# Optimization experiments

Measured on AMD Instinct MI355X. Metric: run time of the kernel, lower is better.

Reference implementation:

```python
import jax, jax.numpy as jnp
import numpy as np

V, BS, L, H, D, DF = 32000, 2048, 4, 4, 256, 1024
B, T = 2, 2048
DH = D // H


def setup_inputs() -> dict:
    key = jax.random.key(0)
    ks = iter(jax.random.split(key, 32))
    s = 0.02
    rn = lambda shape: jax.random.normal(next(ks), shape, jnp.float32) * s
    inp = {
        'idx': jax.random.randint(next(ks), (B, T), 0, V),
        'tok_emb': rn((V, D)),
        'pos_emb': rn((BS, D)),
        'Wq': rn((L, D, D)), 'bq': jnp.zeros((L, D)),
        'Wk': rn((L, D, D)), 'bk': jnp.zeros((L, D)),
        'Wv': rn((L, D, D)), 'bv': jnp.zeros((L, D)),
        'Wo': rn((L, D, D)), 'bo': jnp.zeros((L, D)),
        'ln1_g': jnp.ones((L, D)), 'ln1_b': jnp.zeros((L, D)),
        'W1': rn((L, D, DF)), 'b1': jnp.zeros((L, DF)),
        'W2': rn((L, DF, D)), 'b2': jnp.zeros((L, D)),
        'ln2_g': jnp.ones((L, D)), 'ln2_b': jnp.zeros((L, D)),
        'lnf_g': jnp.ones((D,)), 'lnf_b': jnp.zeros((D,)),
        'head_W': rn((D, V)), 'head_b': jnp.zeros((V,)),
    }
    return inp


def _layernorm(x, g, b, eps=1e-5):
    mu = jnp.mean(x, axis=-1, keepdims=True)
    var = jnp.mean(jnp.square(x - mu), axis=-1, keepdims=True)
    return (x - mu) * jax.lax.rsqrt(var + eps) * g + b


def reference(idx, tok_emb, pos_emb, Wq, bq, Wk, bk, Wv, bv, Wo, bo,
              ln1_g, ln1_b, W1, b1, W2, b2, ln2_g, ln2_b,
              lnf_g, lnf_b, head_W, head_b):
    b, t = idx.shape
    x = tok_emb[idx] + pos_emb[:t]  # [B,T,D]
    causal = jnp.tril(jnp.ones((t, t), dtype=bool))  # [T,T]
    scale = 1.0 / np.sqrt(DH)
    neg_inf = jnp.finfo(x.dtype).min
    for l in range(L):
        h = _layernorm(x, ln1_g[l], ln1_b[l])
        q = (h @ Wq[l] + bq[l]).reshape(b, t, H, DH)
        k = (h @ Wk[l] + bk[l]).reshape(b, t, H, DH)
        v = (h @ Wv[l] + bv[l]).reshape(b, t, H, DH)
        att = jnp.einsum('bqhd,bkhd->bhqk', q, k) * scale
        att = jnp.where(causal, att, neg_inf)
        att = jax.nn.softmax(att, axis=-1)
        y = jnp.einsum('bhqk,bkhd->bqhd', att, v).reshape(b, t, D)
        x = x + (y @ Wo[l] + bo[l])
        h = _layernorm(x, ln2_g[l], ln2_b[l])
        x = x + (jax.nn.gelu(h @ W1[l] + b1[l], approximate=False) @ W2[l] + b2[l])
    x = _layernorm(x, lnf_g, lnf_b)
    return x @ head_W + head_b  # [B,T,V]
```

## Files before the change

kernel.cpp:

```cpp
#include <hip/hip_runtime.h>
#include <hip/hip_bf16.h>
#include <math.h>

#define V_   32000
#define L_   4
#define H_   4
#define D_   256
#define DF_  1024
#define B_   2
#define T_   2048
#define DH_  64
#define NTOK (B_*T_)

typedef __attribute__((ext_vector_type(8))) short bf16x8;
typedef __attribute__((ext_vector_type(4))) float f32x4;
typedef unsigned short u16;

#define GLOAD16(gsrc, ldst) \
  __builtin_amdgcn_global_load_lds((const __attribute__((address_space(1))) void*)(gsrc), \
                                   (__attribute__((address_space(3))) void*)(ldst), 16, 0, 0)

__device__ __forceinline__ u16 f2bf(float f) {
    unsigned int u = __builtin_bit_cast(unsigned int, f);
    u = (u + 0x7fff + ((u >> 16) & 1)) >> 16;
    return (u16)u;
}

__device__ __forceinline__ int xcd_swizzle(int orig, int nwg) {
    return ((nwg & 7) == 0) ? ((orig & 7) * (nwg >> 3) + (orig >> 3)) : orig;
}

__global__ __launch_bounds__(256) void prep_kernel(
    const float* __restrict__ Wq, const float* __restrict__ Wk,
    const float* __restrict__ Wv, const float* __restrict__ Wo,
    const float* __restrict__ W1, const float* __restrict__ W2,
    const float* __restrict__ hW,
    u16* __restrict__ WqkvT, u16* __restrict__ WoT,
    u16* __restrict__ W1T, u16* __restrict__ W2T, u16* __restrict__ hWT)
{
    int b = blockIdx.x;
    const float* src; u16* dst; int K, N, k0, n0;
    if (b < 512) {
        int m = b >> 5, t = b & 31;
        int wt = m & 3, l = m >> 2;
        K = 256; N = 256;
        src = (wt == 0 ? Wq : wt == 1 ? Wk : wt == 2 ? Wv : Wo) + (size_t)l * 65536;
        dst = (wt < 3) ? WqkvT + (size_t)l * 196608 + (size_t)wt * 65536
                       : WoT + (size_t)l * 65536;
        k0 = (t >> 3) * 64; n0 = (t & 7) * 32;
    } else if (b < 1024) {
        int bb = b - 512; int l = bb >> 7, t = bb & 127;
        K = 256; N = 1024;
        src = W1 + (size_t)l * 262144; dst = W1T + (size_t)l * 262144;
        k0 = (t >> 5) * 64; n0 = (t & 31) * 32;
    } else if (b < 1536) {
        int bb = b - 1024; int l = bb >> 7, t = bb & 127;
        K = 1024; N = 256;
        src = W2 + (size_t)l * 262144; dst = W2T + (size_t)l * 262144;
        k0 = (t >> 3) * 64; n0 = (t & 7) * 32;
    } else {
        int bb = b - 1536;
        K = 256; N = 32000;
        src = hW; dst = hWT;
        k0 = (bb / 1000) * 64; n0 = (bb % 1000) * 32;
    }
    __shared__ float tile[64][33];
    int tid = threadIdx.x;
    int tc = tid & 31, tr = tid >> 5;
    #pragma unroll
    for (int i = 0; i < 8; i++)
        tile[tr + i*8][tc] = src[(size_t)(k0 + tr + i*8) * N + n0 + tc];
    __syncthreads();
    int kc = tid & 63, nr = tid >> 6;
    #pragma unroll
    for (int i = 0; i < 8; i++)
        dst[(size_t)(n0 + nr + i*4) * K + k0 + kc] = f2bf(tile[kc][nr + i*4]);
}

__global__ __launch_bounds__(256) void embed_qkv_kernel(
    const int* __restrict__ idx, const float* __restrict__ tok, const float* __restrict__ pos,
    const float* __restrict__ g, const float* __restrict__ bta,
    const u16* __restrict__ WqkvT0,
    const float* __restrict__ bq, const float* __restrict__ bk, const float* __restrict__ bv,
    float* __restrict__ x, u16* __restrict__ qkv)
{
    __shared__ u16 Bs[2][256*64];
    __shared__ u16 hS[16][264];

    int tid = threadIdx.x;
    int lane = tid & 63, w = tid >> 6;
    int lr = lane & 15, lg = lane >> 4;
    int bid = xcd_swizzle(blockIdx.x, 256);
    int row0 = bid * 16;

    {
        int grow = tid >> 4;
        int gcol = (tid & 15) * 16;
        int n = row0 + grow;
        int t = n & (T_ - 1);
        int id = idx[n];
        float vv[16];
        #pragma unroll
        for (int i = 0; i < 4; i++) {
            float4 a = *(const float4*)(tok + (size_t)id * D_ + gcol + i * 4);
            float4 b = *(const float4*)(pos + (size_t)t * D_ + gcol + i * 4);
            vv[i*4+0] = a.x + b.x; vv[i*4+1] = a.y + b.y;
            vv[i*4+2] = a.z + b.z; vv[i*4+3] = a.w + b.w;
        }
        float s = 0.f, q = 0.f;
        #pragma unroll
        for (int i = 0; i < 16; i++) { s += vv[i]; q += vv[i]*vv[i]; }
        #pragma unroll
        for (int o = 1; o <= 8; o <<= 1) { s += __shfl_xor(s, o); q += __shfl_xor(q, o); }
        float mu = s * (1.0f / D_);
        float var = q * (1.0f / D_) - mu * mu;
        float ri = rsqrtf(var + 1e-5f);
        #pragma unroll
        for (int i = 0; i < 16; i++) {
            x[(size_t)n * D_ + gcol + i] = vv[i];
            hS[grow][gcol + i] = f2bf((vv[i] - mu) * ri * g[gcol + i] + bta[gcol + i]);
        }
    }

    auto stageQ = [&](int buf, int u) {
        const u16* BT = WqkvT0 + (size_t)(u >> 2) * 65536;
        int k0 = (u & 3) * 64;
        #pragma unroll
        for (int i = 0; i < 8; i++) {
            int o16 = tid + i * 256;
            int r = o16 >> 3;
            int sw = ((o16 & 7) << 4) ^ ((r & 7) << 4);
            GLOAD16(BT + (size_t)r * 256 + k0 + (sw >> 1), &Bs[buf][o16 * 8]);
        }
    };
    auto afH = [&](int t, int ks) -> bf16x8 {
        return *(const bf16x8*)(&hS[lr][(t * 128 + ks * 64 + lg * 16) >> 1]);
    };
    auto bfr = [&](int buf, int ni, int ks) -> bf16x8 {
        int rr = w * 64 + ni * 16 + lr;
        return *(const bf16x8*)(&Bs[buf][rr * 64 + (((ks * 64 + lg * 16) ^ ((rr & 7) << 4)) >> 1)]);
    };

    stageQ(0, 0);
    f32x4 acc[4] = {};
    for (int u = 0; u < 12; u++) {
        __syncthreads();
        if (u + 1 < 12) stageQ((u + 1) & 1, u + 1);
        int t = u & 3;
        #pragma unroll
        for (int ks = 0; ks < 2; ks++) {
            bf16x8 a = afH(t, ks);
            __builtin_amdgcn_s_setprio(1);
            #pragma unroll
            for (int ni = 0; ni < 4; ni++)
                acc[ni] = __builtin_amdgcn_mfma_f32_16x16x32_bf16(a, bfr(u & 1, ni, ks), acc[ni], 0, 0, 0);
            __builtin_amdgcn_s_setprio(0);
        }
        if (t == 3) {
            int sel = u >> 2;
            const float* bp = sel == 0 ? bq : sel == 1 ? bk : bv;
            #pragma unroll
            for (int ni = 0; ni < 4; ni++) {
                #pragma unroll
                for (int j = 0; j < 4; j++) {
                    int row = row0 + lg * 4 + j;
                    int cc = w * 64 + ni * 16 + lr;
                    float v = acc[ni][j] + bp[cc];
                    int bb = row >> 11, tt = row & (T_ - 1);
                    int hh = cc >> 6, dh = cc & 63;
                    qkv[(size_t)sel * NTOK * D_ +
                        ((((size_t)bb * H_ + hh) * T_) + tt) * DH_ + dh] = f2bf(v);
                }
                acc[ni] = (f32x4){0.f, 0.f, 0.f, 0.f};
            }
        }
    }
}

__global__ __launch_bounds__(256) void wo_ln_kernel(
    const u16* __restrict__ ybuf, const u16* __restrict__ WoT, const float* __restrict__ bo,
    const float* __restrict__ ln2g, const float* __restrict__ ln2b,
    float* __restrict__ x, u16* __restrict__ hbuf)
{
    __shared__ u16 As[2][16*64];
    __shared__ u16 Bs[2][256*64];
    __shared__ float sred[4][16], qred[4][16];

    int tid = threadIdx.x;
    int lane = tid & 63, w = tid >> 6;
    int lr = lane & 15, lg = lane >> 4;
    int bid = xcd_swizzle(blockIdx.x, 256);
    int row0 = bid * 16;

    auto stage = [&](int buf, int k0) {
        #pragma unroll
        for (int i = 0; i < 8; i++) {
            int o16 = tid + i * 256;
            int r = o16 >> 3;
            int sw = ((o16 & 7) << 4) ^ ((r & 7) << 4);
            GLOAD16(WoT + (size_t)r * 256 + k0 + (sw >> 1), &Bs[buf][o16 * 8]);
        }
        if (tid < 128) {
            int r = tid >> 3;
            int sw = ((tid & 7) << 4) ^ ((r & 7) << 4);
            GLOAD16(ybuf + (size_t)(row0 + r) * 256 + k0 + (sw >> 1), &As[buf][tid * 8]);
        }
    };
    auto afA = [&](int buf, int ks) -> bf16x8 {
        return *(const bf16x8*)(&As[buf][lr * 64 + (((ks * 64 + lg * 16) ^ ((lr & 7) << 4)) >> 1)]);
    };
    auto bfr = [&](int buf, int ni, int ks) -> bf16x8 {
        int rr = w * 64 + ni * 16 + lr;
        return *(const bf16x8*)(&Bs[buf][rr * 64 + (((ks * 64 + lg * 16) ^ ((rr & 7) << 4)) >> 1)]);
    };

    stage(0, 0);
    f32x4 acc[4] = {};
    for (int t = 0; t < 4; t++) {
        __syncthreads();
        if (t + 1 < 4) stage((t + 1) & 1, (t + 1) * 64);
        #pragma unroll
        for (int ks = 0; ks < 2; ks++) {
            bf16x8 a = afA(t & 1, ks);
            __builtin_amdgcn_s_setprio(1);
            #pragma unroll
            for (int ni = 0; ni < 4; ni++)
                acc[ni] = __builtin_amdgcn_mfma_f32_16x16x32_bf16(a, bfr(t & 1, ni, ks), acc[ni], 0, 0, 0);
            __builtin_amdgcn_s_setprio(0);
        }
    }

    float vals[4][4];
    float rs[4] = {0,0,0,0}, rq[4] = {0,0,0,0};
    #pragma unroll
    for (int ni = 0; ni < 4; ni++)
        #pragma unroll
        for (int j = 0; j < 4; j++) {
            int row = row0 + lg * 4 + j;
            int col = w * 64 + ni * 16 + lr;
            float v = acc[ni][j] + bo[col] + x[(size_t)row * D_ + col];
            x[(size_t)row * D_ + col] = v;
            vals[ni][j] = v;
            rs[j] += v; rq[j] += v * v;
        }
    #pragma unroll
    for (int j = 0; j < 4; j++)
        #pragma unroll
        for (int o = 1; o <= 8; o <<= 1) { rs[j] += __shfl_xor(rs[j], o); rq[j] += __shfl_xor(rq[j], o); }
    if (lr == 0)
        #pragma unroll
        for (int j = 0; j < 4; j++) { sred[w][lg*4 + j] = rs[j]; qred[w][lg*4 + j] = rq[j]; }
    __syncthreads();
    #pragma unroll
    for (int j = 0; j < 4; j++) {
        int r = lg * 4 + j;
        float mu = (sred[0][r] + sred[1][r] + sred[2][r] + sred[3][r]) * (1.0f / D_);
        float var = (qred[0][r] + qred[1][r] + qred[2][r] + qred[3][r]) * (1.0f / D_) - mu * mu;
        float ri = rsqrtf(var + 1e-5f);
        int row = row0 + r;
        #pragma unroll
        for (int ni = 0; ni < 4; ni++) {
            int col = w * 64 + ni * 16 + lr;
            hbuf[(size_t)row * D_ + col] = f2bf((vals[ni][j] - mu) * ri * ln2g[col] + ln2b[col]);
        }
    }
}

__global__ __launch_bounds__(256) void ff1_kernel(
    const u16* __restrict__ A, const u16* __restrict__ BT,
    const float* __restrict__ bias, u16* __restrict__ C)
{
    __shared__ u16 As[2][64*64];
    __shared__ u16 Bs[2][64*64];
    int tid = threadIdx.x;
    int lane = tid & 63, w = tid >> 6;
    int lr = lane & 15, lg = lane >> 4;
    int wm = w >> 1, wn = w & 1;

    int gx = gridDim.x;
    int nwg = gx * gridDim.y;
    int orig = blockIdx.y * gx + blockIdx.x;
    int bid = xcd_swizzle(orig, nwg);
    int row0 = (bid / gx) * 64, col0 = (bid % gx) * 64;

    auto stage = [&](int buf, int k0) {
        #pragma unroll
        for (int i = 0; i < 2; i++) {
            int o16 = tid + i * 256;
            int r = o16 >> 3;
            int sw = ((o16 & 7) << 4) ^ ((r & 7) << 4);
            GLOAD16(A + (size_t)(row0 + r) * 256 + k0 + (sw >> 1), &As[buf][o16 * 8]);
            GLOAD16(BT + (size_t)(col0 + r) * 256 + k0 + (sw >> 1), &Bs[buf][o16 * 8]);
        }
    };

    stage(0, 0);
    f32x4 acc[2][2] = {};
    for (int t = 0; t < 4; t++) {
        __syncthreads();
        if (t + 1 < 4) stage((t + 1) & 1, (t + 1) * 64);
        #pragma unroll
        for (int ks = 0; ks < 2; ks++) {
            bf16x8 af[2], bfv[2];
            #pragma unroll
            for (int mi = 0; mi < 2; mi++) {
                int rr = wm * 32 + mi * 16 + lr;
                af[mi] = *(const bf16x8*)(&As[t & 1][rr * 64 + (((ks * 64 + lg * 16) ^ ((rr & 7) << 4)) >> 1)]);
            }
            #pragma unroll
            for (int ni = 0; ni < 2; ni++) {
                int rr = wn * 32 + ni * 16 + lr;
                bfv[ni] = *(const bf16x8*)(&Bs[t & 1][rr * 64 + (((ks * 64 + lg * 16) ^ ((rr & 7) << 4)) >> 1)]);
            }
            __builtin_amdgcn_s_setprio(1);
            #pragma unroll
            for (int mi = 0; mi < 2; mi++)
                #pragma unroll
                for (int ni = 0; ni < 2; ni++)
                    acc[mi][ni] = __builtin_amdgcn_mfma_f32_16x16x32_bf16(af[mi], bfv[ni], acc[mi][ni], 0, 0, 0);
            __builtin_amdgcn_s_setprio(0);
        }
    }

    #pragma unroll
    for (int mi = 0; mi < 2; mi++)
        #pragma unroll
        for (int ni = 0; ni < 2; ni++)
            #pragma unroll
            for (int j = 0; j < 4; j++) {
                int row = row0 + wm * 32 + mi * 16 + lg * 4 + j;
                int col = col0 + wn * 32 + ni * 16 + lr;
                float v = acc[mi][ni][j] + bias[col];
                v = 0.5f * v * (1.0f + erff(v * 0.70710678118f));
                C[(size_t)row * DF_ + col] = f2bf(v);
            }
}

template<bool LAST>
__global__ __launch_bounds__(256) void ff2qkv_kernel(
    const u16* __restrict__ ff, const u16* __restrict__ W2T, const float* __restrict__ b2,
    const float* __restrict__ lng, const float* __restrict__ lnb,
    const u16* __restrict__ WqkvT,
    const float* __restrict__ bq, const float* __restrict__ bk, const float* __restrict__ bv,
    float* __restrict__ x, u16* __restrict__ hout, u16* __restrict__ qkv)
{
    __shared__ u16 As[2][16*64];
    __shared__ u16 Bs[2][256*64];
    __shared__ u16 hS[16][264];
    __shared__ float sred[4][16], qred[4][16];

    int tid = threadIdx.x;
    int lane = tid & 63, w = tid >> 6;
    int lr = lane & 15, lg = lane >> 4;
    int bid = xcd_swizzle(blockIdx.x, 256);
    int row0 = bid * 16;

    auto stageB = [&](int buf, const u16* BT, int K, int k0) {
        #pragma unroll
        for (int i = 0; i < 8; i++) {
            int o16 = tid + i * 256;
            int r = o16 >> 3;
            int sw = ((o16 & 7) << 4) ^ ((r & 7) << 4);
            GLOAD16(BT + (size_t)r * K + k0 + (sw >> 1), &Bs[buf][o16 * 8]);
        }
    };
    auto stageA = [&](int buf, int k0) {
        if (tid < 128) {
            int r = tid >> 3;
            int sw = ((tid & 7) << 4) ^ ((r & 7) << 4);
            GLOAD16(ff + (size_t)(row0 + r) * DF_ + k0 + (sw >> 1), &As[buf][tid * 8]);
        }
    };
    auto prefetch = [&](int u) {
        if (u < 16) { stageA(u & 1, u * 64); stageB(u & 1, W2T, 1024, u * 64); }
        else if (!LAST && u < 28) {
            int v = u - 16;
            stageB(u & 1, WqkvT + (size_t)(v >> 2) * 65536, 256, (v & 3) * 64);
        }
    };
    auto afA = [&](int buf, int ks) -> bf16x8 {
        return *(const bf16x8*)(&As[buf][lr * 64 + (((ks * 64 + lg * 16) ^ ((lr & 7) << 4)) >> 1)]);
    };
    auto afH = [&](int t, int ks) -> bf16x8 {
        return *(const bf16x8*)(&hS[lr][(t * 128 + ks * 64 + lg * 16) >> 1]);
    };
    auto bfr = [&](int buf, int ni, int ks) -> bf16x8 {
        int rr = w * 64 + ni * 16 + lr;
        return *(const bf16x8*)(&Bs[buf][rr * 64 + (((ks * 64 + lg * 16) ^ ((rr & 7) << 4)) >> 1)]);
    };

    prefetch(0);
    f32x4 acc[4] = {};
    for (int u = 0; u < 16; u++) {
        __syncthreads();
        prefetch(u + 1);
        #pragma unroll
        for (int ks = 0; ks < 2; ks++) {
            bf16x8 a = afA(u & 1, ks);
            __builtin_amdgcn_s_setprio(1);
            #pragma unroll
            for (int ni = 0; ni < 4; ni++)
                acc[ni] = __builtin_amdgcn_mfma_f32_16x16x32_bf16(a, bfr(u & 1, ni, ks), acc[ni], 0, 0, 0);
            __builtin_amdgcn_s_setprio(0);
        }
    }

    {
        float vals[4][4];
        float rs[4] = {0,0,0,0}, rq[4] = {0,0,0,0};
        #pragma unroll
        for (int ni = 0; ni < 4; ni++)
            #pragma unroll
            for (int j = 0; j < 4; j++) {
                int row = row0 + lg * 4 + j;
                int col = w * 64 + ni * 16 + lr;
                float v = acc[ni][j] + b2[col] + x[(size_t)row * D_ + col];
                x[(size_t)row * D_ + col] = v;
                vals[ni][j] = v;
                rs[j] += v; rq[j] += v * v;
            }
        #pragma unroll
        for (int j = 0; j < 4; j++)
            #pragma unroll
            for (int o = 1; o <= 8; o <<= 1) { rs[j] += __shfl_xor(rs[j], o); rq[j] += __shfl_xor(rq[j], o); }
        if (lr == 0)
            #pragma unroll
            for (int j = 0; j < 4; j++) { sred[w][lg*4 + j] = rs[j]; qred[w][lg*4 + j] = rq[j]; }
        __syncthreads();
        #pragma unroll
        for (int j = 0; j < 4; j++) {
            int r = lg * 4 + j;
            float mu = (sred[0][r] + sred[1][r] + sred[2][r] + sred[3][r]) * (1.0f / D_);
            float var = (qred[0][r] + qred[1][r] + qred[2][r] + qred[3][r]) * (1.0f / D_) - mu * mu;
            float ri = rsqrtf(var + 1e-5f);
            #pragma unroll
            for (int ni = 0; ni < 4; ni++) {
                int col = w * 64 + ni * 16 + lr;
                float hv = (vals[ni][j] - mu) * ri * lng[col] + lnb[col];
                if (LAST) hout[(size_t)(row0 + r) * D_ + col] = f2bf(hv);
                else      hS[r][col] = f2bf(hv);
            }
        }
    }

    if constexpr (!LAST) {
        f32x4 accT[4] = {};
        for (int v = 0; v < 12; v++) {
            __syncthreads();
            prefetch(16 + v + 1);
            int t = v & 3;
            #pragma unroll
            for (int ks = 0; ks < 2; ks++) {
                bf16x8 a = afH(t, ks);
                __builtin_amdgcn_s_setprio(1);
                #pragma unroll
                for (int ni = 0; ni < 4; ni++)
                    accT[ni] = __builtin_amdgcn_mfma_f32_16x16x32_bf16(a, bfr(v & 1, ni, ks), accT[ni], 0, 0, 0);
                __builtin_amdgcn_s_setprio(0);
            }
            if (t == 3) {
                int sel = v >> 2;
                const float* bp = sel == 0 ? bq : sel == 1 ? bk : bv;
                #pragma unroll
                for (int ni = 0; ni < 4; ni++) {
                    #pragma unroll
                    for (int j = 0; j < 4; j++) {
                        int row = row0 + lg * 4 + j;
                        int cc = w * 64 + ni * 16 + lr;
                        float val = accT[ni][j] + bp[cc];
                        int bb = row >> 11, tt = row & (T_ - 1);
                        int hh = cc >> 6, dh = cc & 63;
                        qkv[(size_t)sel * NTOK * D_ +
                            ((((size_t)bb * H_ + hh) * T_) + tt) * DH_ + dh] = f2bf(val);
                    }
                    accT[ni] = (f32x4){0.f, 0.f, 0.f, 0.f};
                }
            }
        }
    }
}

__global__ __launch_bounds__(256) void attn_kernel(
    const u16* __restrict__ q, const u16* __restrict__ k,
    const u16* __restrict__ v, u16* __restrict__ y)
{
    int linear = blockIdx.y * gridDim.x + blockIdx.x;
    int half = linear >> 8, rem = linear & 255;
    int qt_raw = rem & 63;
    int qt = half ? 63 - qt_raw : qt_raw;
    int bh = (rem >> 6) + half * 4;
    int bidx = bh >> 2, h = bh & 3;
    const u16* qp = q + (size_t)bh * T_ * DH_;
    const u16* kp = k + (size_t)bh * T_ * DH_;
    const u16* vp = v + (size_t)bh * T_ * DH_;

    int nch = (qt + 2) >> 1;

    __shared__ u16 Qs[32*64];
    __shared__ u16 Ks[2][2][64*64];
    __shared__ u16 VT[2][64*72];
    __shared__ u16 Ps[4][16*72];

    int tid = threadIdx.x;
    int lane = tid & 63, w = tid >> 6;
    int lr = lane & 15, lg = lane >> 4;
    int p = w >> 1;
    int rh = w & 1;
    int cnt0 = (nch + 1) >> 1, cnt1 = nch >> 1;
    int mycnt = p ? cnt1 : cnt0;
    int maxit = cnt0;

    int pp = tid >> 7;
    int ppcnt = pp ? cnt1 : cnt0;
    int vkey = tid & 63;
    int vdh0 = ((tid >> 6) & 1) * 8;

    {
        int o16 = tid, r = o16 >> 3;
        int sw = ((o16 & 7) << 4) ^ ((r & 7) << 4);
        GLOAD16(qp + (size_t)(qt * 32 + r) * DH_ + (sw >> 1), &Qs[o16 * 8]);
    }
    #pragma unroll
    for (int pr = 0; pr < 2; pr++) {
        int c = min(pr, nch - 1);
        #pragma unroll
        for (int i = 0; i < 2; i++) {
            int o16 = tid + i * 256, r = o16 >> 3;
            int sw = ((o16 & 7) << 4) ^ ((r & 7) << 4);
            GLOAD16(kp + (size_t)(c * 64 + r) * DH_ + (sw >> 1), &Ks[0][pr][o16 * 8]);
        }
    }
    bf16x8 vr[4];
    {
        int c = min(pp, nch - 1);
        #pragma unroll
        for (int g = 0; g < 4; g++)
            vr[g] = *(const bf16x8*)(vp + (size_t)(c * 64 + vkey) * DH_ + vdh0 + g * 16);
    }
    __syncthreads();
    #pragma unroll
    for (int g = 0; g < 4; g++)
        #pragma unroll
        for (int e = 0; e < 8; e++)
            VT[pp][(vdh0 + g * 16 + e) * 72 + vkey] = (u16)vr[g][e];
    bf16x8 qa[2];
    #pragma unroll
    for (int ks = 0; ks < 2; ks++) {
        int rr = rh * 16 + lr;
        qa[ks] = *(const bf16x8*)(Qs + rr * 64 + (((ks * 64 + lg * 16) ^ ((rr & 7) << 4)) >> 1));
    }
    __syncthreads();

    float m[4], lden[4];
    f32x4 o[4] = {};
    #pragma unroll
    for (int j = 0; j < 4; j++) { m[j] = -1e30f; lden[j] = 0.0f; }

    for (int it = 0; it < maxit; it++) {
        int cur = it & 1;
        if (it + 1 < maxit) {
            #pragma unroll
            for (int pr = 0; pr < 2; pr++) {
                int c = min(2 * (it + 1) + pr, nch - 1);
                #pragma unroll
                for (int i = 0; i < 2; i++) {
                    int o16 = tid + i * 256, r = o16 >> 3;
                    int sw = ((o16 & 7) << 4) ^ ((r & 7) << 4);
                    GLOAD16(kp + (size_t)(c * 64 + r) * DH_ + (sw >> 1), &Ks[cur ^ 1][pr][o16 * 8]);
                }
            }
        }
        bool vnext = (it + 1 < ppcnt);
        if (vnext) {
            int c = 2 * (it + 1) + pp;
            #pragma unroll
            for (int g = 0; g < 4; g++)
                vr[g] = *(const bf16x8*)(vp + (size_t)(c * 64 + vkey) * DH_ + vdh0 + g * 16);
        }

        bool act = (it < mycnt);
        if (act) {
            int myc = 2 * it + p;
            f32x4 sc[4];
            #pragma unroll
            for (int ct = 0; ct < 4; ct++) {
                f32x4 s = {};
                __builtin_amdgcn_s_setprio(1);
                #pragma unroll
                for (int ks = 0; ks < 2; ks++) {
                    int rr = ct * 16 + lr;
                    bf16x8 kb = *(const bf16x8*)(&Ks[cur][p][rr * 64 + (((ks * 64 + lg * 16) ^ ((rr & 7) << 4)) >> 1)]);
                    s = __builtin_amdgcn_mfma_f32_16x16x32_bf16(qa[ks], kb, s, 0, 0, 0);
                }
                __builtin_amdgcn_s_setprio(0);
                sc[ct] = s;
            }
            float mloc[4];
            #pragma unroll
            for (int j = 0; j < 4; j++) mloc[j] = -1e30f;
            #pragma unroll
            for (int ct = 0; ct < 4; ct++)
                #pragma unroll
                for (int j = 0; j < 4; j++) {
                    float s = sc[ct][j] * 0.125f;
                    int key = myc * 64 + ct * 16 + lr;
                    int qrow = qt * 32 + rh * 16 + lg * 4 + j;
                    if (key > qrow) s = -1e30f;
                    sc[ct][j] = s;
                    mloc[j] = fmaxf(mloc[j], s);
                }
            #pragma unroll
            for (int j = 0; j < 4; j++) {
                mloc[j] = fmaxf(mloc[j], __shfl_xor(mloc[j], 1));
                mloc[j] = fmaxf(mloc[j], __shfl_xor(mloc[j], 2));
                mloc[j] = fmaxf(mloc[j], __shfl_xor(mloc[j], 4));
                mloc[j] = fmaxf(mloc[j], __shfl_xor(mloc[j], 8));
            }
            float f[4], rs[4];
            #pragma unroll
            for (int j = 0; j < 4; j++) {
                float nm = fmaxf(m[j], mloc[j]);
                f[j] = __expf(m[j] - nm);
                m[j] = nm;
                rs[j] = 0.0f;
            }
            #pragma unroll
            for (int ct = 0; ct < 4; ct++)
                #pragma unroll
                for (int j = 0; j < 4; j++) {
                    float pv = __expf(sc[ct][j] - m[j]);
                    rs[j] += pv;
                    Ps[w][(lg * 4 + j) * 72 + ct * 16 + lr] = f2bf(pv);
                }
            #pragma unroll
            for (int j = 0; j < 4; j++) {
                rs[j] += __shfl_xor(rs[j], 1);
                rs[j] += __shfl_xor(rs[j], 2);
                rs[j] += __shfl_xor(rs[j], 4);
                rs[j] += __shfl_xor(rs[j], 8);
                lden[j] = lden[j] * f[j] + rs[j];
            }
            #pragma unroll
            for (int dt = 0; dt < 4; dt++)
                #pragma unroll
                for (int j = 0; j < 4; j++)
                    o[dt][j] *= f[j];
            #pragma unroll
            for (int ks = 0; ks < 2; ks++) {
                bf16x8 pa = *(const bf16x8*)(&Ps[w][lr * 72 + ks * 32 + lg * 8]);
                __builtin_amdgcn_s_setprio(1);
                #pragma unroll
                for (int dt = 0; dt < 4; dt++) {
                    bf16x8 vb = *(const bf16x8*)(&VT[p][(dt * 16 + lr) * 72 + ks * 32 + lg * 8]);
                    o[dt] = __builtin_amdgcn_mfma_f32_16x16x32_bf16(pa, vb, o[dt], 0, 0, 0);
                }
                __builtin_amdgcn_s_setprio(0);
            }
        }
        __syncthreads();
        if (vnext) {
            #pragma unroll
            for (int g = 0; g < 4; g++)
                #pragma unroll
                for (int e = 0; e < 8; e++)
                    VT[pp][(vdh0 + g * 16 + e) * 72 + vkey] = (u16)vr[g][e];
        }
        __syncthreads();
    }

    float* mg = (float*)&Ks[0][0][0];
    if (p == 1) {
        int base = (rh * 64 + lane) * 24;
        #pragma unroll
        for (int dt = 0; dt < 4; dt++)
            #pragma unroll
            for (int j = 0; j < 4; j++)
                mg[base + dt * 4 + j] = o[dt][j];
        #pragma unroll
        for (int j = 0; j < 4; j++) { mg[base + 16 + j] = m[j]; mg[base + 20 + j] = lden[j]; }
    }
    __syncthreads();
    if (p == 0) {
        int base = (rh * 64 + lane) * 24;
        #pragma unroll
        for (int j = 0; j < 4; j++) {
            float m1 = mg[base + 16 + j];
            float l1 = mg[base + 20 + j];
            float mf = fmaxf(m[j], m1);
            float e0 = __expf(m[j] - mf), e1 = __expf(m1 - mf);
            float inv = 1.0f / (lden[j] * e0 + l1 * e1);
            int qrow = qt * 32 + rh * 16 + lg * 4 + j;
            size_t ybase = ((size_t)(bidx * T_ + qrow)) * D_ + h * DH_;
            #pragma unroll
            for (int dt = 0; dt < 4; dt++) {
                float of = (o[dt][j] * e0 + mg[base + dt * 4 + j] * e1) * inv;
                y[ybase + dt * 16 + lr] = f2bf(of);
            }
        }
    }
}

__global__ __launch_bounds__(256) void head_gemm(
    const u16* __restrict__ A, const u16* __restrict__ BT,
    const float* __restrict__ bias, float* __restrict__ C,
    int M, int N, int K)
{
    __shared__ u16 As[2][128*64];
    __shared__ u16 Bs[2][128*64];
    int tid = threadIdx.x;
    int lane = tid & 63, w = tid >> 6;
    int lr = lane & 15, lg = lane >> 4;
    int wm = w >> 1, wn = w & 1;

    int orig = blockIdx.y * gridDim.x + blockIdx.x;
    int bid = xcd_swizzle(orig, 8000);
    int col0 = (bid >> 5) * 128;
    int row0 = (bid & 31) * 128;

    f32x4 acc[4][4] = {};

    auto stage = [&](int buf, int k0) {
        #pragma unroll
        for (int i = 0; i < 4; i++) {
            int o16 = tid + i * 256;
            int r = o16 >> 3;
            int sw = ((o16 & 7) << 4) ^ ((r & 7) << 4);
            GLOAD16(A + (size_t)(row0 + r) * K + k0 + (sw >> 1), &As[buf][o16 * 8]);
            GLOAD16(BT + (size_t)(col0 + r) * K + k0 + (sw >> 1), &Bs[buf][o16 * 8]);
        }
    };

    stage(0, 0);
    int nk = K >> 6;
    for (int t = 0; t < nk; t++) {
        int cur = t & 1;
        __syncthreads();
        if (t + 1 < nk) stage(cur ^ 1, (t + 1) << 6);
        #pragma unroll
        for (int ks = 0; ks < 2; ks++) {
            bf16x8 af[4], bfr[4];
            #pragma unroll
            for (int mi = 0; mi < 4; mi++) {
                int rr = wm * 64 + mi * 16 + lr;
                af[mi] = *(const bf16x8*)(&As[cur][rr * 64 + (((ks * 64 + lg * 16) ^ ((rr & 7) << 4)) >> 1)]);
            }
            #pragma unroll
            for (int ni = 0; ni < 4; ni++) {
                int rr = wn * 64 + ni * 16 + lr;
                bfr[ni] = *(const bf16x8*)(&Bs[cur][rr * 64 + (((ks * 64 + lg * 16) ^ ((rr & 7) << 4)) >> 1)]);
            }
            __builtin_amdgcn_s_setprio(1);
            #pragma unroll
            for (int mi = 0; mi < 4; mi++)
                #pragma unroll
                for (int ni = 0; ni < 4; ni++)
                    acc[mi][ni] = __builtin_amdgcn_mfma_f32_16x16x32_bf16(af[mi], bfr[ni], acc[mi][ni], 0, 0, 0);
            __builtin_amdgcn_s_setprio(0);
        }
    }

    #pragma unroll
    for (int mi = 0; mi < 4; mi++)
        #pragma unroll
        for (int ni = 0; ni < 4; ni++)
            #pragma unroll
            for (int j = 0; j < 4; j++) {
                int row = row0 + wm * 64 + mi * 16 + lg * 4 + j;
                int col = col0 + wn * 64 + ni * 16 + lr;
                __builtin_nontemporal_store(acc[mi][ni][j] + bias[col], &C[(size_t)row * N + col]);
            }
}

extern "C" void kernel_launch(void* const* d_in, const int* in_sizes, int n_in,
                              void* d_out, int out_size, void* d_ws, size_t ws_size,
                              hipStream_t stream)
{
    const int*   idx  = (const int*)d_in[0];
    const float* tok  = (const float*)d_in[1];
    const float* pos  = (const float*)d_in[2];
    const float* Wq   = (const float*)d_in[3];
    const float* bq   = (const float*)d_in[4];
    const float* Wk   = (const float*)d_in[5];
    const float* bk   = (const float*)d_in[6];
    const float* Wv   = (const float*)d_in[7];
    const float* bv   = (const float*)d_in[8];
    const float* Wo   = (const float*)d_in[9];
    const float* bo   = (const float*)d_in[10];
    const float* ln1g = (const float*)d_in[11];
    const float* ln1b = (const float*)d_in[12];
    const float* W1   = (const float*)d_in[13];
    const float* b1   = (const float*)d_in[14];
    const float* W2   = (const float*)d_in[15];
    const float* b2   = (const float*)d_in[16];
    const float* ln2g = (const float*)d_in[17];
    const float* ln2b = (const float*)d_in[18];
    const float* lnfg = (const float*)d_in[19];
    const float* lnfb = (const float*)d_in[20];
    const float* hW   = (const float*)d_in[21];
    const float* hb   = (const float*)d_in[22];

    char* p = (char*)d_ws;
    float* x     = (float*)p;           p += (size_t)NTOK * D_ * 4;
    u16* hbuf    = (u16*)p;             p += (size_t)NTOK * D_ * 2;
    u16* qkvbuf  = (u16*)p;             p += (size_t)3 * NTOK * D_ * 2;
    u16* ybuf    = (u16*)p;             p += (size_t)NTOK * D_ * 2;
    u16* ff      = (u16*)p;             p += (size_t)NTOK * DF_ * 2;
    u16* WqkvT   = (u16*)p;             p += (size_t)L_ * 768 * D_ * 2;
    u16* WoT     = (u16*)p;             p += (size_t)L_ * D_ * D_ * 2;
    u16* W1T     = (u16*)p;             p += (size_t)L_ * D_ * DF_ * 2;
    u16* W2T     = (u16*)p;             p += (size_t)L_ * DF_ * D_ * 2;
    u16* hWT     = (u16*)p;             p += (size_t)V_ * D_ * 2;

    u16* qbuf = qkvbuf;
    u16* kbuf = qkvbuf + (size_t)NTOK * D_;
    u16* vbuf = qkvbuf + (size_t)2 * NTOK * D_;

    prep_kernel<<<5536, 256, 0, stream>>>(Wq, Wk, Wv, Wo, W1, W2, hW,
                                          WqkvT, WoT, W1T, W2T, hWT);

    embed_qkv_kernel<<<256, 256, 0, stream>>>(idx, tok, pos, ln1g, ln1b,
                                              WqkvT, bq, bk, bv, x, qkvbuf);

    dim3 gAttn(64, 8);
    dim3 gFF1(DF_ / 64, NTOK / 64);
    for (int l = 0; l < L_; l++) {
        attn_kernel<<<gAttn, 256, 0, stream>>>(qbuf, kbuf, vbuf, ybuf);
        wo_ln_kernel<<<256, 256, 0, stream>>>(ybuf, WoT + (size_t)l * 65536, bo + l * D_,
                                              ln2g + l * D_, ln2b + l * D_, x, hbuf);
        ff1_kernel<<<gFF1, 256, 0, stream>>>(hbuf, W1T + (size_t)l * 262144, b1 + l * DF_, ff);
        if (l < L_ - 1) {
            ff2qkv_kernel<false><<<256, 256, 0, stream>>>(
                ff, W2T + (size_t)l * 262144, b2 + l * D_,
                ln1g + (l + 1) * D_, ln1b + (l + 1) * D_,
                WqkvT + (size_t)(l + 1) * 196608,
                bq + (l + 1) * D_, bk + (l + 1) * D_, bv + (l + 1) * D_,
                x, nullptr, qkvbuf);
        } else {
            ff2qkv_kernel<true><<<256, 256, 0, stream>>>(
                ff, W2T + (size_t)l * 262144, b2 + l * D_,
                lnfg, lnfb,
                nullptr, nullptr, nullptr, nullptr,
                x, hbuf, nullptr);
        }
    }

    dim3 gHead(V_ / 128, NTOK / 128);
    head_gemm<<<gHead, 256, 0, stream>>>(hbuf, hWT, hb, (float*)d_out, NTOK, V_, D_);
}
```

Measured before the change: 513.7 us.

## Fuse Wo projection, LayerNorm2 and FF1 GEMM into one kernel

Merges the Wo+residual+LN2 kernel with the FF1+GELU GEMM so each 16-row block keeps the normalized activations in shared memory and streams all four 256-column chunks of W1 through a continuous double-buffered prefetch. This removes one kernel launch per layer and the global round trip of the normalized hidden buffer. In exchange, FF1 now runs on only 256 blocks with 16-row tiles instead of 1024 blocks with 64x64 tiles. Each block also re-reads the full W1 matrix, which lowers parallelism and raises L2 weight traffic.

```diff
diff --git a/kernel.cpp b/kernel.cpp
--- a/kernel.cpp
+++ b/kernel.cpp
@@ -177,13 +177,16 @@
     }
 }
 
-__global__ __launch_bounds__(256) void wo_ln_kernel(
-    const u16* __restrict__ ybuf, const u16* __restrict__ WoT, const float* __restrict__ bo,
+__global__ __launch_bounds__(256) void woff1_kernel(
+    const u16* __restrict__ ybuf,
+    const u16* __restrict__ WoT, const float* __restrict__ bo,
+    const u16* __restrict__ W1T, const float* __restrict__ b1,
     const float* __restrict__ ln2g, const float* __restrict__ ln2b,
-    float* __restrict__ x, u16* __restrict__ hbuf)
+    float* __restrict__ x, u16* __restrict__ ff)
 {
+    __shared__ u16 Bs[2][256*64];
     __shared__ u16 As[2][16*64];
-    __shared__ u16 Bs[2][256*64];
+    __shared__ u16 hS[16][264];
     __shared__ float sred[4][16], qred[4][16];
 
     int tid = threadIdx.x;
@@ -192,148 +195,123 @@
     int bid = xcd_swizzle(blockIdx.x, 256);
     int row0 = bid * 16;
 
-    auto stage = [&](int buf, int k0) {
+    auto stageB = [&](int buf, const u16* BT, int k0) {
         #pragma unroll
         for (int i = 0; i < 8; i++) {
             int o16 = tid + i * 256;
             int r = o16 >> 3;
             int sw = ((o16 & 7) << 4) ^ ((r & 7) << 4);
-            GLOAD16(WoT + (size_t)r * 256 + k0 + (sw >> 1), &Bs[buf][o16 * 8]);
-        }
+            GLOAD16(BT + (size_t)r * 256 + k0 + (sw >> 1), &Bs[buf][o16 * 8]);
+        }
+    };
+    auto stageA = [&](int buf, int k0) {
         if (tid < 128) {
             int r = tid >> 3;
             int sw = ((tid & 7) << 4) ^ ((r & 7) << 4);
             GLOAD16(ybuf + (size_t)(row0 + r) * 256 + k0 + (sw >> 1), &As[buf][tid * 8]);
         }
     };
+    auto prefetch = [&](int u) {
+        int buf = u & 1;
+        if (u < 4)       { stageA(buf, u * 64); stageB(buf, WoT, u * 64); }
+        else if (u < 20) { int v = u - 4; stageB(buf, W1T + (size_t)(v >> 2) * 65536, (v & 3) * 64); }
+    };
     auto afA = [&](int buf, int ks) -> bf16x8 {
         return *(const bf16x8*)(&As[buf][lr * 64 + (((ks * 64 + lg * 16) ^ ((lr & 7) << 4)) >> 1)]);
+    };
+    auto afH = [&](int t, int ks) -> bf16x8 {
+        return *(const bf16x8*)(&hS[lr][(t * 128 + ks * 64 + lg * 16) >> 1]);
     };
     auto bfr = [&](int buf, int ni, int ks) -> bf16x8 {
         int rr = w * 64 + ni * 16 + lr;
         return *(const bf16x8*)(&Bs[buf][rr * 64 + (((ks * 64 + lg * 16) ^ ((rr & 7) << 4)) >> 1)]);
     };
 
-    stage(0, 0);
-    f32x4 acc[4] = {};
-    for (int t = 0; t < 4; t++) {
+    prefetch(0);
+
+    {
+        f32x4 acc[4] = {};
+        for (int u = 0; u < 4; u++) {
+            __syncthreads();
+            prefetch(u + 1);
+            #pragma unroll
+            for (int ks = 0; ks < 2; ks++) {
+                bf16x8 a = afA(u & 1, ks);
+                __builtin_amdgcn_s_setprio(1);
+                #pragma unroll
+                for (int ni = 0; ni < 4; ni++)
+                    acc[ni] = __builtin_amdgcn_mfma_f32_16x16x32_bf16(a, bfr(u & 1, ni, ks), acc[ni], 0, 0, 0);
+                __builtin_amdgcn_s_setprio(0);
+            }
+        }
+        float vals[4][4];
+        float rs[4] = {0,0,0,0}, rq[4] = {0,0,0,0};
+        #pragma unroll
+        for (int ni = 0; ni < 4; ni++)
+            #pragma unroll
+            for (int j = 0; j < 4; j++) {
+                int row = row0 + lg * 4 + j;
+                int col = w * 64 + ni * 16 + lr;
+                float v = acc[ni][j] + bo[col] + x[(size_t)row * D_ + col];
+                x[(size_t)row * D_ + col] = v;
+                vals[ni][j] = v;
+                rs[j] += v; rq[j] += v * v;
+            }
+        #pragma unroll
+        for (int j = 0; j < 4; j++)
+            #pragma unroll
+            for (int o = 1; o <= 8; o <<= 1) { rs[j] += __shfl_xor(rs[j], o); rq[j] += __shfl_xor(rq[j], o); }
+        if (lr == 0)
+            #pragma unroll
+            for (int j = 0; j < 4; j++) { sred[w][lg*4 + j] = rs[j]; qred[w][lg*4 + j] = rq[j]; }
         __syncthreads();
-        if (t + 1 < 4) stage((t + 1) & 1, (t + 1) * 64);
-        #pragma unroll
-        for (int ks = 0; ks < 2; ks++) {
-            bf16x8 a = afA(t & 1, ks);
-            __builtin_amdgcn_s_setprio(1);
-            #pragma unroll
-            for (int ni = 0; ni < 4; ni++)
-                acc[ni] = __builtin_amdgcn_mfma_f32_16x16x32_bf16(a, bfr(t & 1, ni, ks), acc[ni], 0, 0, 0);
-            __builtin_amdgcn_s_setprio(0);
-        }
-    }
-
-    float vals[4][4];
-    float rs[4] = {0,0,0,0}, rq[4] = {0,0,0,0};
-    #pragma unroll
-    for (int ni = 0; ni < 4; ni++)
         #pragma unroll
         for (int j = 0; j < 4; j++) {
-            int row = row0 + lg * 4 + j;
-            int col = w * 64 + ni * 16 + lr;
-            float v = acc[ni][j] + bo[col] + x[(size_t)row * D_ + col];
-            x[(size_t)row * D_ + col] = v;
-            vals[ni][j] = v;
-            rs[j] += v; rq[j] += v * v;
-        }
-    #pragma unroll
-    for (int j = 0; j < 4; j++)
-        #pragma unroll
-        for (int o = 1; o <= 8; o <<= 1) { rs[j] += __shfl_xor(rs[j], o); rq[j] += __shfl_xor(rq[j], o); }
-    if (lr == 0)
-        #pragma unroll
-        for (int j = 0; j < 4; j++) { sred[w][lg*4 + j] = rs[j]; qred[w][lg*4 + j] = rq[j]; }
-    __syncthreads();
-    #pragma unroll
-    for (int j = 0; j < 4; j++) {
-        int r = lg * 4 + j;
-        float mu = (sred[0][r] + sred[1][r] + sred[2][r] + sred[3][r]) * (1.0f / D_);
-        float var = (qred[0][r] + qred[1][r] + qred[2][r] + qred[3][r]) * (1.0f / D_) - mu * mu;
-        float ri = rsqrtf(var + 1e-5f);
-        int row = row0 + r;
-        #pragma unroll
-        for (int ni = 0; ni < 4; ni++) {
-            int col = w * 64 + ni * 16 + lr;
-            hbuf[(size_t)row * D_ + col] = f2bf((vals[ni][j] - mu) * ri * ln2g[col] + ln2b[col]);
-        }
-    }
-}
-
-__global__ __launch_bounds__(256) void ff1_kernel(
-    const u16* __restrict__ A, const u16* __restrict__ BT,
-    const float* __restrict__ bias, u16* __restrict__ C)
-{
-    __shared__ u16 As[2][64*64];
-    __shared__ u16 Bs[2][64*64];
-    int tid = threadIdx.x;
-    int lane = tid & 63, w = tid >> 6;
-    int lr = lane & 15, lg = lane >> 4;
-    int wm = w >> 1, wn = w & 1;
-
-    int gx = gridDim.x;
-    int nwg = gx * gridDim.y;
-    int orig = blockIdx.y * gx + blockIdx.x;
-    int bid = xcd_swizzle(orig, nwg);
-    int row0 = (bid / gx) * 64, col0 = (bid % gx) * 64;
-
-    auto stage = [&](int buf, int k0) {
-        #pragma unroll
-        for (int i = 0; i < 2; i++) {
-            int o16 = tid + i * 256;
-            int r = o16 >> 3;
-            int sw = ((o16 & 7) << 4) ^ ((r & 7) << 4);
-            GLOAD16(A + (size_t)(row0 + r) * 256 + k0 + (sw >> 1), &As[buf][o16 * 8]);
-            GLOAD16(BT + (size_t)(col0 + r) * 256 + k0 + (sw >> 1), &Bs[buf][o16 * 8]);
-        }
-    };
-
-    stage(0, 0);
-    f32x4 acc[2][2] = {};
-    for (int t = 0; t < 4; t++) {
-        __syncthreads();
-        if (t + 1 < 4) stage((t + 1) & 1, (t + 1) * 64);
-        #pragma unroll
-        for (int ks = 0; ks < 2; ks++) {
-            bf16x8 af[2], bfv[2];
-            #pragma unroll
-            for (int mi = 0; mi < 2; mi++) {
-                int rr = wm * 32 + mi * 16 + lr;
-                af[mi] = *(const bf16x8*)(&As[t & 1][rr * 64 + (((ks * 64 + lg * 16) ^ ((rr & 7) << 4)) >> 1)]);
-            }
-            #pragma unroll
-            for (int ni = 0; ni < 2; ni++) {
-                int rr = wn * 32 + ni * 16 + lr;
-                bfv[ni] = *(const bf16x8*)(&Bs[t & 1][rr * 64 + (((ks * 64 + lg * 16) ^ ((rr & 7) << 4)) >> 1)]);
-            }
-            __builtin_amdgcn_s_setprio(1);
-            #pragma unroll
-            for (int mi = 0; mi < 2; mi++)
-                #pragma unroll
-                for (int ni = 0; ni < 2; ni++)
-                    acc[mi][ni] = __builtin_amdgcn_mfma_f32_16x16x32_bf16(af[mi], bfv[ni], acc[mi][ni], 0, 0, 0);
-            __builtin_amdgcn_s_setprio(0);
-        }
-    }
-
-    #pragma unroll
-    for (int mi = 0; mi < 2; mi++)
-        #pragma unroll
-        for (int ni = 0; ni < 2; ni++)
-            #pragma unroll
-            for (int j = 0; j < 4; j++) {
-                int row = row0 + wm * 32 + mi * 16 + lg * 4 + j;
-                int col = col0 + wn * 32 + ni * 16 + lr;
-                float v = acc[mi][ni][j] + bias[col];
-                v = 0.5f * v * (1.0f + erff(v * 0.70710678118f));
-                C[(size_t)row * DF_ + col] = f2bf(v);
-            }
+            int r = lg * 4 + j;
+            float mu = (sred[0][r] + sred[1][r] + sred[2][r] + sred[3][r]) * (1.0f / D_);
+            float var = (qred[0][r] + qred[1][r] + qred[2][r] + qred[3][r]) * (1.0f / D_) - mu * mu;
+            float ri = rsqrtf(var + 1e-5f);
+            #pragma unroll
+            for (int ni = 0; ni < 4; ni++) {
+                int col = w * 64 + ni * 16 + lr;
+                hS[r][col] = f2bf((vals[ni][j] - mu) * ri * ln2g[col] + ln2b[col]);
+            }
+        }
+    }
+
+    {
+        f32x4 acc[4] = {};
+        for (int u = 4; u < 20; u++) {
+            __syncthreads();
+            prefetch(u + 1);
+            int v = u - 4;
+            int t = v & 3;
+            #pragma unroll
+            for (int ks = 0; ks < 2; ks++) {
+                bf16x8 a = afH(t, ks);
+                __builtin_amdgcn_s_setprio(1);
+                #pragma unroll
+                for (int ni = 0; ni < 4; ni++)
+                    acc[ni] = __builtin_amdgcn_mfma_f32_16x16x32_bf16(a, bfr(u & 1, ni, ks), acc[ni], 0, 0, 0);
+                __builtin_amdgcn_s_setprio(0);
+            }
+            if (t == 3) {
+                int c = v >> 2;
+                #pragma unroll
+                for (int ni = 0; ni < 4; ni++) {
+                    #pragma unroll
+                    for (int j = 0; j < 4; j++) {
+                        int row = row0 + lg * 4 + j;
+                        int col = w * 64 + ni * 16 + lr;
+                        float vv = acc[ni][j] + b1[c * 256 + col];
+                        vv = 0.5f * vv * (1.0f + erff(vv * 0.70710678118f));
+                        ff[(size_t)row * DF_ + c * 256 + col] = f2bf(vv);
+                    }
+                    acc[ni] = (f32x4){0.f, 0.f, 0.f, 0.f};
+                }
+            }
+        }
+    }
 }
 
 template<bool LAST>
@@ -822,12 +800,11 @@
                                               WqkvT, bq, bk, bv, x, qkvbuf);
 
     dim3 gAttn(64, 8);
-    dim3 gFF1(DF_ / 64, NTOK / 64);
     for (int l = 0; l < L_; l++) {
         attn_kernel<<<gAttn, 256, 0, stream>>>(qbuf, kbuf, vbuf, ybuf);
-        wo_ln_kernel<<<256, 256, 0, stream>>>(ybuf, WoT + (size_t)l * 65536, bo + l * D_,
-                                              ln2g + l * D_, ln2b + l * D_, x, hbuf);
-        ff1_kernel<<<gFF1, 256, 0, stream>>>(hbuf, W1T + (size_t)l * 262144, b1 + l * DF_, ff);
+        woff1_kernel<<<256, 256, 0, stream>>>(ybuf, WoT + (size_t)l * 65536, bo + l * D_,
+                                              W1T + (size_t)l * 262144, b1 + l * DF_,
+                                              ln2g + l * D_, ln2b + l * D_, x, ff);
         if (l < L_ - 1) {
             ff2qkv_kernel<false><<<256, 256, 0, stream>>>(
                 ff, W2T + (size_t)l * 262144, b2 + l * D_,
```

New measurement: 657.9 us. +28.1%, slower.
